# Optimization experiments

Hardware: AMD Instinct MI355X
Metric: run time of the kernel (lower is better)

## Reference

```python
import jax, jax.numpy as jnp
import numpy as np
from itertools import combinations

ADD = 4  # max subset size (init kwarg `add`)


def build_mask(n, add):
    # Binary membership mask [S, n], rows in itertools.combinations order
    # for subset sizes 2..add (matches the torch concatenation order).
    rows = []
    for i in range(2, add + 1):
        for c in combinations(range(n), i):
            r = np.zeros(n, dtype=np.float32)
            r[list(c)] = 1.0
            rows.append(r)
    return np.stack(rows)


def setup_inputs() -> dict:
    key = jax.random.key(0)
    kx, _ = jax.random.split(key)
    B, N = 32768, 16
    # inputs must be strictly inside (0,1) so (1/x - 1) > 0
    x = jax.random.uniform(kx, (B, N), dtype=jnp.float32, minval=0.05, maxval=0.95)
    lam = jnp.asarray(0.3, dtype=jnp.float32)
    return {"x": x, "lam": lam}


def reference(x, lam):
    n = x.shape[1]
    M = jnp.asarray(build_mask(n, ADD))  # [S, n]
    # Dombi t-norm is associative: folding pairwise
    #   h <- 1/(1 + ((1/h-1)^lam + (1/x_i-1)^lam)^(1/lam))
    # equals h_c = 1/(1 + (sum_{j in c} (1/x_j - 1)^lam)^(1/lam)).
    t = (1.0 / x - 1.0) ** lam                 # [B, n]
    s = jnp.einsum('bn,sn->bs', t, M)          # subset sums [B, S]
    h = 1.0 / (1.0 + s ** (1.0 / lam))         # [B, S]
    return jnp.concatenate([x, h], axis=1)     # [B, n + S]
```

## Files before the change

kernel.cpp:

```cpp
#include <hip/hip_runtime.h>

#define NSUB  2500
#define NCOL  2516
#define NROW  16
#define NQUAD 625
#define NPAIR 120

struct SubTable { unsigned char idx[NSUB][2]; };
struct PairTable { unsigned char pr[NPAIR][2]; };

constexpr SubTable make_table() {
    SubTable tb{};
    int pidx[16][16] = {};
    {
        int p = 0;
        for (int i = 0; i < 16; ++i)
            for (int j = i + 1; j < 16; ++j) pidx[i][j] = p++;
    }
    int s = 0;
    for (int i = 0; i < 16; ++i)
        for (int j = i + 1; j < 16; ++j) {
            tb.idx[s][0] = (unsigned char)(17 + pidx[i][j]);
            tb.idx[s][1] = 16;  ++s;
        }
    for (int i = 0; i < 16; ++i)
        for (int j = i + 1; j < 16; ++j)
            for (int k = j + 1; k < 16; ++k) {
                tb.idx[s][0] = (unsigned char)(17 + pidx[i][j]);
                tb.idx[s][1] = (unsigned char)k;  ++s;
            }
    for (int i = 0; i < 16; ++i)
        for (int j = i + 1; j < 16; ++j)
            for (int k = j + 1; k < 16; ++k)
                for (int l = k + 1; l < 16; ++l) {
                    tb.idx[s][0] = (unsigned char)(17 + pidx[i][j]);
                    tb.idx[s][1] = (unsigned char)(17 + pidx[k][l]);  ++s;
                }
    return tb;
}

constexpr PairTable make_pairs() {
    PairTable t{};
    int p = 0;
    for (int i = 0; i < 16; ++i)
        for (int j = i + 1; j < 16; ++j) {
            t.pr[p][0] = (unsigned char)i;
            t.pr[p][1] = (unsigned char)j;  ++p;
        }
    return t;
}

__constant__ SubTable  g_tab = make_table();
__constant__ PairTable g_pr  = make_pairs();

typedef float         f32x4 __attribute__((ext_vector_type(4)));
typedef unsigned char u8x8  __attribute__((ext_vector_type(8)));

__device__ __forceinline__ float hval(float s, float p) {
    float q = __builtin_amdgcn_logf(s);
    float e = __builtin_amdgcn_exp2f(p * q);
    return __builtin_amdgcn_rcpf(1.0f + e);
}

__global__ __launch_bounds__(256) void dombi_kernel(const float* __restrict__ x,
                                                    const float* __restrict__ lam_p,
                                                    float* __restrict__ out) {
    __shared__ float tt[137];
    const int   row     = blockIdx.x;
    const int   tid     = threadIdx.x;
    const float lam     = lam_p[0];
    const float inv_lam = 1.0f / lam;

    const float* xr   = x   + (size_t)row * NROW;
    float*       orow = out + (size_t)row * NCOL;

    if (tid < NROW) {
        float xv = xr[tid];
        tt[tid] = powf(1.0f / xv - 1.0f, lam);
    } else if (tid == NROW) {
        tt[NROW] = 0.0f;
    }
    if (tid < 4) {
        reinterpret_cast<f32x4*>(orow)[tid] =
            reinterpret_cast<const f32x4*>(xr)[tid];
    }
    __syncthreads();

    if (tid < NPAIR) {
        tt[17 + tid] = tt[g_pr.pr[tid][0]] + tt[g_pr.pr[tid][1]];
    }
    __syncthreads();

    const u8x8* cp = reinterpret_cast<const u8x8*>(&g_tab.idx[0][0]);
    f32x4*      o4 = reinterpret_cast<f32x4*>(orow + NROW);

    for (int s4 = tid; s4 < NQUAD; s4 += 256) {
        u8x8 c = cp[s4];
        f32x4 r;
        r.x = hval(tt[c[0]] + tt[c[1]], inv_lam);
        r.y = hval(tt[c[2]] + tt[c[3]], inv_lam);
        r.z = hval(tt[c[4]] + tt[c[5]], inv_lam);
        r.w = hval(tt[c[6]] + tt[c[7]], inv_lam);
        __builtin_nontemporal_store(r, &o4[s4]);
    }
}

extern "C" void kernel_launch(void* const* d_in, const int* in_sizes, int n_in,
                              void* d_out, int out_size, void* d_ws, size_t ws_size,
                              hipStream_t stream) {
    const float* x   = (const float*)d_in[0];
    const float* lam = (const float*)d_in[1];
    float*       out = (float*)d_out;
    const int B = in_sizes[0] / NROW;
    dombi_kernel<<<B, 256, 0, stream>>>(x, lam, out);
}
```

Baseline: 358.8 us.

## Process eight rows per block with two rows per wave sharing index loads

Each block now handles eight batch rows instead of one, and each wavefront computes two rows per iteration so every subset-index table load is reused for both. This amortizes the per-row setup and synchronization and removes the partly idle 256-thread loop over 625 quads. The grid launch assumes the batch size is a multiple of eight, and the fixed 10-iteration loop leaves some lanes idle on the last pass.

```diff
diff --git a/kernel.cpp b/kernel.cpp
--- a/kernel.cpp
+++ b/kernel.cpp
@@ -5,8 +5,10 @@
 #define NROW  16
 #define NQUAD 625
 #define NPAIR 120
+#define RPB   8
+#define TSTR  137
 
-struct SubTable { unsigned char idx[NSUB][2]; };
+struct SubTable  { unsigned char idx[NSUB][2]; };
 struct PairTable { unsigned char pr[NPAIR][2]; };
 
 constexpr SubTable make_table() {
@@ -62,46 +64,60 @@
     return __builtin_amdgcn_rcpf(1.0f + e);
 }
 
-__global__ __launch_bounds__(256) void dombi_kernel(const float* __restrict__ x,
-                                                    const float* __restrict__ lam_p,
-                                                    float* __restrict__ out) {
-    __shared__ float tt[137];
-    const int   row     = blockIdx.x;
+__global__ __launch_bounds__(256, 4) void dombi_kernel(const float* __restrict__ x,
+                                                       const float* __restrict__ lam_p,
+                                                       float* __restrict__ out) {
+    __shared__ float tt[RPB][TSTR];
     const int   tid     = threadIdx.x;
+    const int   row0    = blockIdx.x * RPB;
     const float lam     = lam_p[0];
     const float inv_lam = 1.0f / lam;
 
-    const float* xr   = x   + (size_t)row * NROW;
-    float*       orow = out + (size_t)row * NCOL;
+    const float* xb = x + (size_t)row0 * NROW;
 
-    if (tid < NROW) {
-        float xv = xr[tid];
-        tt[tid] = powf(1.0f / xv - 1.0f, lam);
-    } else if (tid == NROW) {
-        tt[NROW] = 0.0f;
-    }
-    if (tid < 4) {
-        reinterpret_cast<f32x4*>(orow)[tid] =
-            reinterpret_cast<const f32x4*>(xr)[tid];
+    if (tid < RPB * NROW) {
+        float xv = xb[tid];
+        int r = tid >> 4, j = tid & 15;
+        out[(size_t)(row0 + r) * NCOL + j] = xv;
+        tt[r][j] = powf(1.0f / xv - 1.0f, lam);
+        if (j == 0) tt[r][16] = 0.0f;
     }
     __syncthreads();
 
-    if (tid < NPAIR) {
-        tt[17 + tid] = tt[g_pr.pr[tid][0]] + tt[g_pr.pr[tid][1]];
+    for (int k = tid; k < RPB * NPAIR; k += 256) {
+        int r = k / NPAIR;
+        int p = k - r * NPAIR;
+        tt[r][17 + p] = tt[r][g_pr.pr[p][0]] + tt[r][g_pr.pr[p][1]];
     }
     __syncthreads();
 
+    const int wave = tid >> 6;
+    const int lane = tid & 63;
+    const int rA   = wave * 2;
+    const int rB   = rA + 1;
     const u8x8* cp = reinterpret_cast<const u8x8*>(&g_tab.idx[0][0]);
-    f32x4*      o4 = reinterpret_cast<f32x4*>(orow + NROW);
+    f32x4* oA = reinterpret_cast<f32x4*>(out + (size_t)(row0 + rA) * NCOL + NROW);
+    f32x4* oB = reinterpret_cast<f32x4*>(out + (size_t)(row0 + rB) * NCOL + NROW);
 
-    for (int s4 = tid; s4 < NQUAD; s4 += 256) {
-        u8x8 c = cp[s4];
-        f32x4 r;
-        r.x = hval(tt[c[0]] + tt[c[1]], inv_lam);
-        r.y = hval(tt[c[2]] + tt[c[3]], inv_lam);
-        r.z = hval(tt[c[4]] + tt[c[5]], inv_lam);
-        r.w = hval(tt[c[6]] + tt[c[7]], inv_lam);
-        __builtin_nontemporal_store(r, &o4[s4]);
+#pragma unroll
+    for (int it = 0; it < 10; ++it) {
+        const int  q   = it * 64 + lane;
+        const bool act = (q < NQUAD);
+        const int  qc  = act ? q : NQUAD - 1;
+        u8x8 c = cp[qc];
+        f32x4 vA, vB;
+        vA.x = hval(tt[rA][c[0]] + tt[rA][c[1]], inv_lam);
+        vA.y = hval(tt[rA][c[2]] + tt[rA][c[3]], inv_lam);
+        vA.z = hval(tt[rA][c[4]] + tt[rA][c[5]], inv_lam);
+        vA.w = hval(tt[rA][c[6]] + tt[rA][c[7]], inv_lam);
+        vB.x = hval(tt[rB][c[0]] + tt[rB][c[1]], inv_lam);
+        vB.y = hval(tt[rB][c[2]] + tt[rB][c[3]], inv_lam);
+        vB.z = hval(tt[rB][c[4]] + tt[rB][c[5]], inv_lam);
+        vB.w = hval(tt[rB][c[6]] + tt[rB][c[7]], inv_lam);
+        if (act) {
+            __builtin_nontemporal_store(vA, &oA[q]);
+            __builtin_nontemporal_store(vB, &oB[q]);
+        }
     }
 }
 
@@ -112,5 +128,5 @@
     const float* lam = (const float*)d_in[1];
     float*       out = (float*)d_out;
     const int B = in_sizes[0] / NROW;
-    dombi_kernel<<<B, 256, 0, stream>>>(x, lam, out);
+    dombi_kernel<<<B / RPB, 256, 0, stream>>>(x, lam, out);
 }
```

Result: no change. 357.7 us (-0.3%).
